# Kernel tuning notes

Measured on AMD Instinct MI355X. Metric: run time of the kernel, lower is better.

## Reference

```python
import jax, jax.numpy as jnp
import numpy as np

B, D, O, E, H, K = 4096, 1024, 1024, 8, 4096, 2


def setup_inputs() -> dict:
    key = jax.random.key(0)
    ks = jax.random.split(key, 5)
    scale_g = 1.0 / np.sqrt(D)
    scale_1 = 1.0 / np.sqrt(D)
    scale_2 = 1.0 / np.sqrt(H)
    return {
        "x": jax.random.normal(ks[0], (B, D), jnp.float32),
        "gate_w": jax.random.normal(ks[1], (D, E), jnp.float32) * scale_g,
        "gate_b": jnp.zeros((E,), jnp.float32),
        "w1": jax.random.normal(ks[2], (E, D, H), jnp.float32) * scale_1,
        "b1": jnp.zeros((E, H), jnp.float32),
        "w2": jax.random.normal(ks[3], (E, H, O), jnp.float32) * scale_2,
        "b2": jnp.zeros((E, O), jnp.float32),
    }


def reference(x, gate_w, gate_b, w1, b1, w2, b2):
    # Router: top-k logits, softmax over the k selected logits only
    logits = x @ gate_w + gate_b                      # [B, E]
    top_vals, top_idx = jax.lax.top_k(logits, K)      # [B, K]
    routing_w = jax.nn.softmax(top_vals, axis=-1)     # [B, K]

    # Dense all-expert MLP (grouped GEMM), then gather the k selected outputs
    h = jax.nn.relu(jnp.einsum("bd,edh->beh", x, w1) + b1)  # [B, E, H]
    y = jnp.einsum("beh,eho->beo", h, w2) + b2              # [B, E, O]
    sel = jnp.take_along_axis(y, top_idx[:, :, None], axis=1)  # [B, K, O]
    return jnp.sum(routing_w[:, :, None] * sel, axis=1)        # [B, O]
```

## Files before the change

kernel.cpp:

```cpp
#include <hip/hip_runtime.h>
#include <stdint.h>

typedef short bf16x8 __attribute__((ext_vector_type(8)));
typedef float f32x4  __attribute__((ext_vector_type(4)));

constexpr int BT = 4096;
constexpr int DD = 1024;
constexpr int OO = 1024;
constexpr int EE = 8;
constexpr int HH = 4096;
constexpr int SLOTS = 2 * BT;

constexpr int BM = 128, BN = 128, BK = 32;
constexpr int A_USH = BM * BK;
constexpr int SLOT_USH = (BM + BN) * BK;
constexpr int MTS = 32;
constexpr int G1_BLKS = 8 * 32 * MTS;
constexpr int G2_BLKS = 8 * 2 * 8 * MTS;

__device__ __forceinline__ unsigned short f2bf(float f) {
  unsigned u = __float_as_uint(f);
  u += 0x7fffu + ((u >> 16) & 1u);
  return (unsigned short)(u >> 16);
}

__device__ __forceinline__ void glds16(const unsigned short* g, unsigned short* l) {
  __builtin_amdgcn_global_load_lds(
      (const __attribute__((address_space(1))) void*)g,
      (__attribute__((address_space(3))) void*)l, 16, 0, 0);
}

__device__ __forceinline__ void cvt_body(const float* __restrict__ src,
                                         unsigned short* __restrict__ dst,
                                         int R, int C, int e, int r0, int c0, int t,
                                         unsigned short (*tile)[66]) {
  const float* s = src + (size_t)e * R * C;
  unsigned short* d = dst + (size_t)e * R * C;
#pragma unroll
  for (int p = 0; p < 4; ++p) {
    int ch = p * 256 + t;
    int rr = ch >> 4, cc = (ch & 15) << 2;
    float4 v = *(const float4*)&s[(size_t)(r0 + rr) * C + c0 + cc];
    unsigned lo = (unsigned)f2bf(v.x) | ((unsigned)f2bf(v.y) << 16);
    unsigned hi = (unsigned)f2bf(v.z) | ((unsigned)f2bf(v.w) << 16);
    *(uint2*)&tile[rr][cc] = make_uint2(lo, hi);
  }
  __syncthreads();
#pragma unroll
  for (int p = 0; p < 4; ++p) {
    int ch = p * 256 + t;
    int cc = ch >> 4, rr = (ch & 15) << 2;
    unsigned short v0 = tile[rr + 0][cc];
    unsigned short v1 = tile[rr + 1][cc];
    unsigned short v2 = tile[rr + 2][cc];
    unsigned short v3 = tile[rr + 3][cc];
    unsigned lo = (unsigned)v0 | ((unsigned)v1 << 16);
    unsigned hi = (unsigned)v2 | ((unsigned)v3 << 16);
    *(uint2*)&d[(size_t)(c0 + cc) * R + r0 + rr] = make_uint2(lo, hi);
  }
}

__global__ __launch_bounds__(256) void fusedA_k(const float* __restrict__ x,
                                                const float* __restrict__ gw,
                                                const float* __restrict__ gb,
                                                const float* __restrict__ w1,
                                                unsigned short* __restrict__ xb,
                                                int* __restrict__ cnt,
                                                int* __restrict__ list,
                                                float* __restrict__ rw,
                                                unsigned short* __restrict__ w1t) {
  __shared__ unsigned short tile[64][66];
  int bid = blockIdx.x;
  if (bid >= 1024) {
    int idx = bid - 1024;
    int e = idx >> 10, rem = idx & 1023;
    int r0 = (rem & 15) << 6, c0 = (rem >> 4) << 6;
    cvt_body(w1, w1t, DD, HH, e, r0, c0, threadIdx.x, tile);
    return;
  }
  int wave = threadIdx.x >> 6, lane = threadIdx.x & 63;
  int b = bid * 4 + wave;
  const float* xrow = x + (size_t)b * DD;
  float acc[8];
#pragma unroll
  for (int e = 0; e < 8; ++e) acc[e] = 0.f;
#pragma unroll
  for (int i = 0; i < 4; ++i) {
    int d0 = i * 256 + lane * 4;
    float4 v = *(const float4*)&xrow[d0];
    unsigned lo = (unsigned)f2bf(v.x) | ((unsigned)f2bf(v.y) << 16);
    unsigned hi = (unsigned)f2bf(v.z) | ((unsigned)f2bf(v.w) << 16);
    *(uint2*)&xb[(size_t)b * DD + d0] = make_uint2(lo, hi);
    const float* g0 = &gw[(size_t)d0 * 8];
    float fv[4] = {v.x, v.y, v.z, v.w};
#pragma unroll
    for (int q = 0; q < 4; ++q) {
      float4 ga = *(const float4*)&g0[q * 8];
      float4 gc = *(const float4*)&g0[q * 8 + 4];
      acc[0] += fv[q] * ga.x; acc[1] += fv[q] * ga.y;
      acc[2] += fv[q] * ga.z; acc[3] += fv[q] * ga.w;
      acc[4] += fv[q] * gc.x; acc[5] += fv[q] * gc.y;
      acc[6] += fv[q] * gc.z; acc[7] += fv[q] * gc.w;
    }
  }
#pragma unroll
  for (int off = 32; off > 0; off >>= 1) {
#pragma unroll
    for (int e = 0; e < 8; ++e) acc[e] += __shfl_down(acc[e], off);
  }
  if (lane == 0) {
    float v[8];
#pragma unroll
    for (int e = 0; e < 8; ++e) v[e] = acc[e] + gb[e];
    int i0 = 0;
#pragma unroll
    for (int e = 1; e < 8; ++e) if (v[e] > v[i0]) i0 = e;
    int i1 = (i0 == 0) ? 1 : 0;
#pragma unroll
    for (int e = 0; e < 8; ++e) if (e != i0 && v[e] > v[i1]) i1 = e;
    float e1 = __expf(v[i1] - v[i0]);
    float inv = 1.0f / (1.0f + e1);
    int p0 = atomicAdd(&cnt[i0], 1);
    list[i0 * BT + p0] = 2 * b;     rw[2 * b]     = inv;
    int p1 = atomicAdd(&cnt[i1], 1);
    list[i1 * BT + p1] = 2 * b + 1; rw[2 * b + 1] = e1 * inv;
  }
}

__global__ void tilemap_k(const int* __restrict__ cnt, int* __restrict__ tmap,
                          int* __restrict__ ntiles, int* __restrict__ tstart) {
  if (threadIdx.x == 0 && blockIdx.x == 0) {
    int t = 0, basewalk = 0;
    for (int e = 0; e < EE; ++e) {
      tstart[e] = t;
      int c = cnt[e];
      for (int m0 = 0; m0 < c; m0 += BM) {
        tmap[4 * t] = e; tmap[4 * t + 1] = m0; tmap[4 * t + 2] = basewalk + m0; ++t;
      }
      basewalk += c;
    }
    tstart[EE] = t;
    *ntiles = t;
  }
}

__global__ __launch_bounds__(256) void cvt_t_k(const float* __restrict__ src,
                                               unsigned short* __restrict__ dst,
                                               int R, int C) {
  __shared__ unsigned short tile[64][66];
  cvt_body(src, dst, R, C, blockIdx.z, blockIdx.x << 6, blockIdx.y << 6,
           threadIdx.x, tile);
}

__global__ __launch_bounds__(256, 3) void fusedB_k(const unsigned short* __restrict__ xb,
                                                   const unsigned short* __restrict__ w1t,
                                                   const float* __restrict__ b1,
                                                   const int* __restrict__ cnt,
                                                   const int* __restrict__ list,
                                                   const int* __restrict__ tmap,
                                                   const int* __restrict__ tstart,
                                                   unsigned short* __restrict__ hc,
                                                   const float* __restrict__ w2,
                                                   unsigned short* __restrict__ w2t) {
  __shared__ __align__(16) unsigned short lds[3 * SLOT_USH];
  __shared__ int slotbuf[BM];
  int bid = blockIdx.x;
  if (bid >= G1_BLKS) {
    int idx = bid - G1_BLKS;
    int e = idx >> 10, rem = idx & 1023;
    int r0 = (rem & 63) << 6, c0 = (rem >> 6) << 6;
    cvt_body(w2, w2t, HH, OO, e, r0, c0, threadIdx.x,
             (unsigned short (*)[66])lds);
    return;
  }
  int q = bid & 7, r = bid >> 3;
  int mts = r & (MTS - 1), nt = r >> 5;
  int tc0 = tstart[q];
  if (tc0 + mts >= tstart[q + 1]) return;
  int ti = tc0 + mts;
  int e = tmap[4 * ti], m0 = tmap[4 * ti + 1], base = tmap[4 * ti + 2];
  int cnt_e = cnt[e];
  int n0 = nt * BN;

  int t = threadIdx.x;
  if (t < BM) {
    int rr = m0 + t;
    slotbuf[t] = list[e * BT + (rr < cnt_e ? rr : 0)];
  }
  __syncthreads();

  int w = t >> 6, l = t & 63, lm = l & 15, lq = l >> 4;
  int wm = (w >> 1) * 64, wn = (w & 1) * 64;

  const unsigned short* aS[2];
  const unsigned short* bS[2];
  int dA[2], dB[2];
#pragma unroll
  for (int j = 0; j < 2; ++j) {
    int row = w * 32 + j * 16 + (l >> 2);
    int sch = ((l & 3) ^ ((row >> 1) & 3)) * 8;
    aS[j] = xb + (size_t)(slotbuf[row] >> 1) * DD + sch;
    bS[j] = w1t + (size_t)e * HH * DD + (size_t)(n0 + row) * DD + sch;
    dA[j] = w * 1024 + j * 512;
    dB[j] = A_USH + w * 1024 + j * 512;
  }

  int xs = (lq ^ ((lm >> 1) & 3)) * 8;
  int afo[4], bfo[4];
#pragma unroll
  for (int mi = 0; mi < 4; ++mi) afo[mi] = (wm + mi * 16 + lm) * BK + xs;
#pragma unroll
  for (int ni = 0; ni < 4; ++ni) bfo[ni] = A_USH + (wn + ni * 16 + lm) * BK + xs;

  f32x4 acc[4][4];
#pragma unroll
  for (int mi = 0; mi < 4; ++mi)
#pragma unroll
    for (int ni = 0; ni < 4; ++ni) acc[mi][ni] = f32x4{0.f, 0.f, 0.f, 0.f};

  constexpr int NT = DD / BK;

#pragma unroll
  for (int p = 0; p < 2; ++p) {
    unsigned short* Lb = lds + p * SLOT_USH;
    glds16(aS[0] + p * BK, Lb + dA[0]);
    glds16(aS[1] + p * BK, Lb + dA[1]);
    glds16(bS[0] + p * BK, Lb + dB[0]);
    glds16(bS[1] + p * BK, Lb + dB[1]);
  }
  asm volatile("s_waitcnt vmcnt(4)" ::: "memory");
  __builtin_amdgcn_s_barrier();
  asm volatile("" ::: "memory");

  int sc = 0, ss = 2;
  for (int tt = 0; tt < NT; ++tt) {
    {
      int ts = tt + 2;
      int ko = (ts < NT ? ts : NT - 1) * BK;
      unsigned short* Lb = lds + ss * SLOT_USH;
      glds16(aS[0] + ko, Lb + dA[0]);
      glds16(aS[1] + ko, Lb + dA[1]);
      glds16(bS[0] + ko, Lb + dB[0]);
      glds16(bS[1] + ko, Lb + dB[1]);
    }
    const unsigned short* Lc = lds + sc * SLOT_USH;
    bf16x8 af[4], bf[4];
#pragma unroll
    for (int mi = 0; mi < 4; ++mi) af[mi] = *(const bf16x8*)&Lc[afo[mi]];
#pragma unroll
    for (int ni = 0; ni < 4; ++ni) bf[ni] = *(const bf16x8*)&Lc[bfo[ni]];
    __builtin_amdgcn_s_setprio(1);
#pragma unroll
    for (int mi = 0; mi < 4; ++mi)
#pragma unroll
      for (int ni = 0; ni < 4; ++ni)
        acc[mi][ni] = __builtin_amdgcn_mfma_f32_16x16x32_bf16(af[mi], bf[ni], acc[mi][ni], 0, 0, 0);
    __builtin_amdgcn_s_setprio(0);
    asm volatile("s_waitcnt vmcnt(4)" ::: "memory");
    __builtin_amdgcn_s_barrier();
    asm volatile("" ::: "memory");
    if (++sc == 3) sc = 0;
    if (++ss == 3) ss = 0;
  }

  asm volatile("s_waitcnt vmcnt(0)" ::: "memory");
  __builtin_amdgcn_s_barrier();
  asm volatile("" ::: "memory");
  unsigned short* cb = lds + w * 4096;
  float bias[4];
#pragma unroll
  for (int ni = 0; ni < 4; ++ni) bias[ni] = b1[e * HH + n0 + wn + ni * 16 + lm];
#pragma unroll
  for (int mi = 0; mi < 4; ++mi)
#pragma unroll
    for (int ni = 0; ni < 4; ++ni)
#pragma unroll
      for (int rr = 0; rr < 4; ++rr)
        cb[(mi * 16 + lq * 4 + rr) * 64 + ni * 16 + lm] =
            f2bf(fmaxf(acc[mi][ni][rr] + bias[ni], 0.0f));
  asm volatile("s_waitcnt lgkmcnt(0)" ::: "memory");
#pragma unroll
  for (int it = 0; it < 8; ++it) {
    int rr = it * 8 + (l >> 3), chk = l & 7;
    int grow = wm + rr;
    if (m0 + grow < cnt_e) {
      uint4 v = *(const uint4*)&cb[rr * 64 + chk * 8];
      *(uint4*)&hc[(size_t)(base + grow) * HH + n0 + wn + chk * 8] = v;
    }
  }
}

__global__ __launch_bounds__(256, 3) void gemm2_k(const unsigned short* __restrict__ hc,
                                                  const unsigned short* __restrict__ w2t,
                                                  const float* __restrict__ b2,
                                                  const int* __restrict__ cnt,
                                                  const int* __restrict__ list,
                                                  const int* __restrict__ tmap,
                                                  const int* __restrict__ tstart,
                                                  const float* __restrict__ rw,
                                                  float* __restrict__ ybuf,
                                                  float* __restrict__ out) {
  int q = blockIdx.x & 7, r = blockIdx.x >> 3;
  int z = r >> 8, s = r & 255;
  int mts = s & (MTS - 1), nt = s >> 5;
  int tc0 = tstart[q];
  if (tc0 + mts >= tstart[q + 1]) return;
  int ti = tc0 + mts;
  int e = tmap[4 * ti], m0 = tmap[4 * ti + 1], base = tmap[4 * ti + 2];
  int cnt_e = cnt[e];
  int n0 = nt * BN;
  int kb0 = z * (HH / 2);
  constexpr int NT = (HH / 2) / BK;

  __shared__ __align__(16) unsigned short lds[3 * SLOT_USH];
  __shared__ int slotbuf[BM];
  __shared__ float rwbuf[BM];

  int t = threadIdx.x;
  if (t < BM) {
    int rr = m0 + t;
    int s_ = list[e * BT + (rr < cnt_e ? rr : 0)];
    slotbuf[t] = s_;
    rwbuf[t] = rw[s_];
  }
  __syncthreads();

  int w = t >> 6, l = t & 63, lm = l & 15, lq = l >> 4;
  int wm = (w >> 1) * 64, wn = (w & 1) * 64;

  const unsigned short* aS[2];
  const unsigned short* bS[2];
  int dA[2], dB[2];
#pragma unroll
  for (int j = 0; j < 2; ++j) {
    int row = w * 32 + j * 16 + (l >> 2);
    int sch = ((l & 3) ^ ((row >> 1) & 3)) * 8;
    int gr = base + row; if (gr > SLOTS - 1) gr = SLOTS - 1;
    aS[j] = hc + (size_t)gr * HH + kb0 + sch;
    bS[j] = w2t + (size_t)e * OO * HH + (size_t)(n0 + row) * HH + kb0 + sch;
    dA[j] = w * 1024 + j * 512;
    dB[j] = A_USH + w * 1024 + j * 512;
  }

  int xs = (lq ^ ((lm >> 1) & 3)) * 8;
  int afo[4], bfo[4];
#pragma unroll
  for (int mi = 0; mi < 4; ++mi) afo[mi] = (wm + mi * 16 + lm) * BK + xs;
#pragma unroll
  for (int ni = 0; ni < 4; ++ni) bfo[ni] = A_USH + (wn + ni * 16 + lm) * BK + xs;

  f32x4 acc[4][4];
#pragma unroll
  for (int mi = 0; mi < 4; ++mi)
#pragma unroll
    for (int ni = 0; ni < 4; ++ni) acc[mi][ni] = f32x4{0.f, 0.f, 0.f, 0.f};

#pragma unroll
  for (int p = 0; p < 2; ++p) {
    unsigned short* Lb = lds + p * SLOT_USH;
    glds16(aS[0] + p * BK, Lb + dA[0]);
    glds16(aS[1] + p * BK, Lb + dA[1]);
    glds16(bS[0] + p * BK, Lb + dB[0]);
    glds16(bS[1] + p * BK, Lb + dB[1]);
  }
  asm volatile("s_waitcnt vmcnt(4)" ::: "memory");
  __builtin_amdgcn_s_barrier();
  asm volatile("" ::: "memory");

  int sc = 0, ss = 2;
  for (int tt = 0; tt < NT; ++tt) {
    {
      int ts = tt + 2;
      int ko = (ts < NT ? ts : NT - 1) * BK;
      unsigned short* Lb = lds + ss * SLOT_USH;
      glds16(aS[0] + ko, Lb + dA[0]);
      glds16(aS[1] + ko, Lb + dA[1]);
      glds16(bS[0] + ko, Lb + dB[0]);
      glds16(bS[1] + ko, Lb + dB[1]);
    }
    const unsigned short* Lc = lds + sc * SLOT_USH;
    bf16x8 af[4], bf[4];
#pragma unroll
    for (int mi = 0; mi < 4; ++mi) af[mi] = *(const bf16x8*)&Lc[afo[mi]];
#pragma unroll
    for (int ni = 0; ni < 4; ++ni) bf[ni] = *(const bf16x8*)&Lc[bfo[ni]];
    __builtin_amdgcn_s_setprio(1);
#pragma unroll
    for (int mi = 0; mi < 4; ++mi)
#pragma unroll
      for (int ni = 0; ni < 4; ++ni)
        acc[mi][ni] = __builtin_amdgcn_mfma_f32_16x16x32_bf16(af[mi], bf[ni], acc[mi][ni], 0, 0, 0);
    __builtin_amdgcn_s_setprio(0);
    asm volatile("s_waitcnt vmcnt(4)" ::: "memory");
    __builtin_amdgcn_s_barrier();
    asm volatile("" ::: "memory");
    if (++sc == 3) sc = 0;
    if (++ss == 3) ss = 0;
  }
  asm volatile("s_waitcnt vmcnt(0)" ::: "memory");

  bool addb = (z == 0);
  size_t ybase = (size_t)z * SLOTS;
#pragma unroll
  for (int ni = 0; ni < 4; ++ni) {
    int ncol = n0 + wn + ni * 16 + lm;
    float bias = addb ? b2[e * OO + ncol] : 0.0f;
#pragma unroll
    for (int mi = 0; mi < 4; ++mi)
#pragma unroll
      for (int rr = 0; rr < 4; ++rr) {
        int lrow = wm + mi * 16 + lq * 4 + rr;
        if (m0 + lrow < cnt_e) {
          float v = (acc[mi][ni][rr] + bias) * rwbuf[lrow];
          int slot = slotbuf[lrow];
          if (ybuf) ybuf[(ybase + slot) * OO + ncol] = v;
          else      atomicAdd(&out[(size_t)(slot >> 1) * OO + ncol], v);
        }
      }
  }
}

__global__ __launch_bounds__(256) void combine_k(const float* __restrict__ y,
                                                 float* __restrict__ out, int nz) {
  int i = blockIdx.x * 256 + threadIdx.x;
  int b = i >> 8, c = i & 255;
  f32x4 acc = {0.f, 0.f, 0.f, 0.f};
  for (int z = 0; z < nz; ++z) {
#pragma unroll
    for (int k = 0; k < 2; ++k) {
      const float4 v = *(const float4*)&y[((size_t)z * SLOTS + 2 * b + k) * OO + c * 4];
      acc[0] += v.x; acc[1] += v.y; acc[2] += v.z; acc[3] += v.w;
    }
  }
  *(f32x4*)&out[(size_t)b * OO + c * 4] = acc;
}

extern "C" void kernel_launch(void* const* d_in, const int* in_sizes, int n_in,
                              void* d_out, int out_size, void* d_ws, size_t ws_size,
                              hipStream_t stream) {
  const float* x  = (const float*)d_in[0];
  const float* gw = (const float*)d_in[1];
  const float* gb = (const float*)d_in[2];
  const float* w1 = (const float*)d_in[3];
  const float* b1 = (const float*)d_in[4];
  const float* w2 = (const float*)d_in[5];
  const float* b2 = (const float*)d_in[6];
  float* out = (float*)d_out;
  char* ws = (char*)d_ws;

  int*            cnt    = (int*)(ws);
  int*            ntiles = (int*)(ws + 64);
  int*            tmap   = (int*)(ws + 128);
  int*            tstart = (int*)(ws + 2560);
  float*          rw     = (float*)(ws + 4096);
  int*            list   = (int*)(ws + (64u << 10));
  unsigned short* xb     = (unsigned short*)(ws + (1u  << 20));
  unsigned short* w1t    = (unsigned short*)(ws + (9u  << 20));

  bool roomy = ws_size >= (201u << 20);
  hipMemsetAsync(cnt, 0, 64, stream);

  if (roomy) {
    unsigned short* w2t = (unsigned short*)(ws + (73u  << 20));
    unsigned short* hc  = (unsigned short*)(ws + (137u << 20));
    float*          ybuf = (float*)(ws + (9u << 20));

    fusedA_k<<<1024 + 8192, 256, 0, stream>>>(x, gw, gb, w1, xb, cnt, list, rw, w1t);
    tilemap_k<<<1, 64, 0, stream>>>(cnt, tmap, ntiles, tstart);
    fusedB_k<<<G1_BLKS + 8192, 256, 0, stream>>>(xb, w1t, b1, cnt, list, tmap, tstart,
                                                 hc, w2, w2t);
    gemm2_k<<<G2_BLKS, 256, 0, stream>>>(hc, w2t, b2, cnt, list, tmap,
                                         tstart, rw, ybuf, out);
    combine_k<<<BT * OO / 1024, 256, 0, stream>>>(ybuf, out, 2);
  } else {
    if (ws_size < (137u << 20)) return;
    unsigned short* w2t = w1t;
    unsigned short* hc  = (unsigned short*)(ws + (73u << 20));
    hipMemsetAsync(out, 0, (size_t)BT * OO * sizeof(float), stream);
    fusedA_k<<<1024 + 8192, 256, 0, stream>>>(x, gw, gb, w1, xb, cnt, list, rw, w1t);
    tilemap_k<<<1, 64, 0, stream>>>(cnt, tmap, ntiles, tstart);
    fusedB_k<<<G1_BLKS, 256, 0, stream>>>(xb, w1t, b1, cnt, list, tmap, tstart,
                                          hc, w2, w2t);
    cvt_t_k<<<dim3(HH / 64, OO / 64, EE), 256, 0, stream>>>(w2, w2t, HH, OO);
    gemm2_k<<<G2_BLKS, 256, 0, stream>>>(hc, w2t, b2, cnt, list, tmap,
                                         tstart, rw, nullptr, out);
  }
}
```

Measured before the change: 642.8 us.

## Batch weight-convert blocks four tiles each and switch GEMMs to double buffering

Each weight-conversion block now handles four 64x64 tiles, issuing all 16 float4 loads up front before transposing through LDS. This cuts the conversion grid fourfold and puts more loads in flight per thread. Both grouped GEMM kernels drop from a three-slot LDS pipeline with prefetch distance two to a two-slot double buffer with vmcnt(0) waits, and raise launch bounds from 3 to 4 blocks per CU. The aim is higher occupancy from lower LDS use, at the cost of less latency hiding per wave and more register pressure in the converter.

Result: no change. 638.7 us (-0.6%).

```diff
diff --git a/kernel.cpp b/kernel.cpp
--- a/kernel.cpp
+++ b/kernel.cpp
@@ -30,33 +30,46 @@
       (__attribute__((address_space(3))) void*)l, 16, 0, 0);
 }
 
-__device__ __forceinline__ void cvt_body(const float* __restrict__ src,
-                                         unsigned short* __restrict__ dst,
-                                         int R, int C, int e, int r0, int c0, int t,
-                                         unsigned short (*tile)[66]) {
+__device__ __forceinline__ void cvt_body4(const float* __restrict__ src,
+                                          unsigned short* __restrict__ dst,
+                                          int R, int C, int e, int r0, int c0, int t,
+                                          unsigned short (*tile)[66]) {
   const float* s = src + (size_t)e * R * C;
   unsigned short* d = dst + (size_t)e * R * C;
-#pragma unroll
-  for (int p = 0; p < 4; ++p) {
-    int ch = p * 256 + t;
-    int rr = ch >> 4, cc = (ch & 15) << 2;
-    float4 v = *(const float4*)&s[(size_t)(r0 + rr) * C + c0 + cc];
-    unsigned lo = (unsigned)f2bf(v.x) | ((unsigned)f2bf(v.y) << 16);
-    unsigned hi = (unsigned)f2bf(v.z) | ((unsigned)f2bf(v.w) << 16);
-    *(uint2*)&tile[rr][cc] = make_uint2(lo, hi);
-  }
-  __syncthreads();
-#pragma unroll
-  for (int p = 0; p < 4; ++p) {
-    int ch = p * 256 + t;
-    int cc = ch >> 4, rr = (ch & 15) << 2;
-    unsigned short v0 = tile[rr + 0][cc];
-    unsigned short v1 = tile[rr + 1][cc];
-    unsigned short v2 = tile[rr + 2][cc];
-    unsigned short v3 = tile[rr + 3][cc];
-    unsigned lo = (unsigned)v0 | ((unsigned)v1 << 16);
-    unsigned hi = (unsigned)v2 | ((unsigned)v3 << 16);
-    *(uint2*)&d[(size_t)(c0 + cc) * R + r0 + rr] = make_uint2(lo, hi);
+  float4 v[16];
+#pragma unroll
+  for (int u = 0; u < 4; ++u)
+#pragma unroll
+    for (int p = 0; p < 4; ++p) {
+      int ch = p * 256 + t;
+      int rr = ch >> 4, cc = (ch & 15) << 2;
+      v[u * 4 + p] = *(const float4*)&s[(size_t)(r0 + rr) * C + c0 + u * 64 + cc];
+    }
+#pragma unroll
+  for (int u = 0; u < 4; ++u) {
+#pragma unroll
+    for (int p = 0; p < 4; ++p) {
+      int ch = p * 256 + t;
+      int rr = ch >> 4, cc = (ch & 15) << 2;
+      float4 q = v[u * 4 + p];
+      unsigned lo = (unsigned)f2bf(q.x) | ((unsigned)f2bf(q.y) << 16);
+      unsigned hi = (unsigned)f2bf(q.z) | ((unsigned)f2bf(q.w) << 16);
+      *(uint2*)&tile[rr][cc] = make_uint2(lo, hi);
+    }
+    __syncthreads();
+#pragma unroll
+    for (int p = 0; p < 4; ++p) {
+      int ch = p * 256 + t;
+      int cc = ch >> 4, rr = (ch & 15) << 2;
+      unsigned short v0 = tile[rr + 0][cc];
+      unsigned short v1 = tile[rr + 1][cc];
+      unsigned short v2 = tile[rr + 2][cc];
+      unsigned short v3 = tile[rr + 3][cc];
+      unsigned lo = (unsigned)v0 | ((unsigned)v1 << 16);
+      unsigned hi = (unsigned)v2 | ((unsigned)v3 << 16);
+      *(uint2*)&d[(size_t)(c0 + u * 64 + cc) * R + r0 + rr] = make_uint2(lo, hi);
+    }
+    __syncthreads();
   }
 }
 
@@ -73,9 +86,9 @@
   int bid = blockIdx.x;
   if (bid >= 1024) {
     int idx = bid - 1024;
-    int e = idx >> 10, rem = idx & 1023;
-    int r0 = (rem & 15) << 6, c0 = (rem >> 4) << 6;
-    cvt_body(w1, w1t, DD, HH, e, r0, c0, threadIdx.x, tile);
+    int e = idx >> 8, rem = idx & 255;
+    int r0 = (rem & 15) << 6, c0 = (rem >> 4) << 8;
+    cvt_body4(w1, w1t, DD, HH, e, r0, c0, threadIdx.x, tile);
     return;
   }
   int wave = threadIdx.x >> 6, lane = threadIdx.x & 63;
@@ -148,11 +161,11 @@
                                                unsigned short* __restrict__ dst,
                                                int R, int C) {
   __shared__ unsigned short tile[64][66];
-  cvt_body(src, dst, R, C, blockIdx.z, blockIdx.x << 6, blockIdx.y << 6,
-           threadIdx.x, tile);
-}
-
-__global__ __launch_bounds__(256, 3) void fusedB_k(const unsigned short* __restrict__ xb,
+  cvt_body4(src, dst, R, C, blockIdx.z, blockIdx.x << 6, blockIdx.y << 8,
+            threadIdx.x, tile);
+}
+
+__global__ __launch_bounds__(256, 4) void fusedB_k(const unsigned short* __restrict__ xb,
                                                    const unsigned short* __restrict__ w1t,
                                                    const float* __restrict__ b1,
                                                    const int* __restrict__ cnt,
@@ -162,15 +175,15 @@
                                                    unsigned short* __restrict__ hc,
                                                    const float* __restrict__ w2,
                                                    unsigned short* __restrict__ w2t) {
-  __shared__ __align__(16) unsigned short lds[3 * SLOT_USH];
+  __shared__ __align__(16) unsigned short lds[2 * SLOT_USH];
   __shared__ int slotbuf[BM];
   int bid = blockIdx.x;
   if (bid >= G1_BLKS) {
     int idx = bid - G1_BLKS;
-    int e = idx >> 10, rem = idx & 1023;
-    int r0 = (rem & 63) << 6, c0 = (rem >> 6) << 6;
-    cvt_body(w2, w2t, HH, OO, e, r0, c0, threadIdx.x,
-             (unsigned short (*)[66])lds);
+    int e = idx >> 8, rem = idx & 255;
+    int r0 = (rem & 63) << 6, c0 = (rem >> 6) << 8;
+    cvt_body4(w2, w2t, HH, OO, e, r0, c0, threadIdx.x,
+              (unsigned short (*)[66])lds);
     return;
   }
   int q = bid & 7, r = bid >> 3;
@@ -220,30 +233,24 @@
 
   constexpr int NT = DD / BK;
 
-#pragma unroll
-  for (int p = 0; p < 2; ++p) {
-    unsigned short* Lb = lds + p * SLOT_USH;
-    glds16(aS[0] + p * BK, Lb + dA[0]);
-    glds16(aS[1] + p * BK, Lb + dA[1]);
-    glds16(bS[0] + p * BK, Lb + dB[0]);
-    glds16(bS[1] + p * BK, Lb + dB[1]);
-  }
-  asm volatile("s_waitcnt vmcnt(4)" ::: "memory");
+  {
+    unsigned short* Lb = lds;
+    glds16(aS[0], Lb + dA[0]); glds16(aS[1], Lb + dA[1]);
+    glds16(bS[0], Lb + dB[0]); glds16(bS[1], Lb + dB[1]);
+  }
+  asm volatile("s_waitcnt vmcnt(0)" ::: "memory");
   __builtin_amdgcn_s_barrier();
   asm volatile("" ::: "memory");
 
-  int sc = 0, ss = 2;
   for (int tt = 0; tt < NT; ++tt) {
     {
-      int ts = tt + 2;
+      int ts = tt + 1;
       int ko = (ts < NT ? ts : NT - 1) * BK;
-      unsigned short* Lb = lds + ss * SLOT_USH;
-      glds16(aS[0] + ko, Lb + dA[0]);
-      glds16(aS[1] + ko, Lb + dA[1]);
-      glds16(bS[0] + ko, Lb + dB[0]);
-      glds16(bS[1] + ko, Lb + dB[1]);
-    }
-    const unsigned short* Lc = lds + sc * SLOT_USH;
+      unsigned short* Lb = lds + (ts & 1) * SLOT_USH;
+      glds16(aS[0] + ko, Lb + dA[0]); glds16(aS[1] + ko, Lb + dA[1]);
+      glds16(bS[0] + ko, Lb + dB[0]); glds16(bS[1] + ko, Lb + dB[1]);
+    }
+    const unsigned short* Lc = lds + (tt & 1) * SLOT_USH;
     bf16x8 af[4], bf[4];
 #pragma unroll
     for (int mi = 0; mi < 4; ++mi) af[mi] = *(const bf16x8*)&Lc[afo[mi]];
@@ -256,16 +263,11 @@
       for (int ni = 0; ni < 4; ++ni)
         acc[mi][ni] = __builtin_amdgcn_mfma_f32_16x16x32_bf16(af[mi], bf[ni], acc[mi][ni], 0, 0, 0);
     __builtin_amdgcn_s_setprio(0);
-    asm volatile("s_waitcnt vmcnt(4)" ::: "memory");
+    asm volatile("s_waitcnt vmcnt(0)" ::: "memory");
     __builtin_amdgcn_s_barrier();
     asm volatile("" ::: "memory");
-    if (++sc == 3) sc = 0;
-    if (++ss == 3) ss = 0;
-  }
-
-  asm volatile("s_waitcnt vmcnt(0)" ::: "memory");
-  __builtin_amdgcn_s_barrier();
-  asm volatile("" ::: "memory");
+  }
+
   unsigned short* cb = lds + w * 4096;
   float bias[4];
 #pragma unroll
@@ -290,7 +292,7 @@
   }
 }
 
-__global__ __launch_bounds__(256, 3) void gemm2_k(const unsigned short* __restrict__ hc,
+__global__ __launch_bounds__(256, 4) void gemm2_k(const unsigned short* __restrict__ hc,
                                                   const unsigned short* __restrict__ w2t,
                                                   const float* __restrict__ b2,
                                                   const int* __restrict__ cnt,
@@ -312,7 +314,7 @@
   int kb0 = z * (HH / 2);
   constexpr int NT = (HH / 2) / BK;
 
-  __shared__ __align__(16) unsigned short lds[3 * SLOT_USH];
+  __shared__ __align__(16) unsigned short lds[2 * SLOT_USH];
   __shared__ int slotbuf[BM];
   __shared__ float rwbuf[BM];
 
@@ -355,30 +357,24 @@
 #pragma unroll
     for (int ni = 0; ni < 4; ++ni) acc[mi][ni] = f32x4{0.f, 0.f, 0.f, 0.f};
 
-#pragma unroll
-  for (int p = 0; p < 2; ++p) {
-    unsigned short* Lb = lds + p * SLOT_USH;
-    glds16(aS[0] + p * BK, Lb + dA[0]);
-    glds16(aS[1] + p * BK, Lb + dA[1]);
-    glds16(bS[0] + p * BK, Lb + dB[0]);
-    glds16(bS[1] + p * BK, Lb + dB[1]);
-  }
-  asm volatile("s_waitcnt vmcnt(4)" ::: "memory");
+  {
+    unsigned short* Lb = lds;
+    glds16(aS[0], Lb + dA[0]); glds16(aS[1], Lb + dA[1]);
+    glds16(bS[0], Lb + dB[0]); glds16(bS[1], Lb + dB[1]);
+  }
+  asm volatile("s_waitcnt vmcnt(0)" ::: "memory");
   __builtin_amdgcn_s_barrier();
   asm volatile("" ::: "memory");
 
-  int sc = 0, ss = 2;
   for (int tt = 0; tt < NT; ++tt) {
     {
-      int ts = tt + 2;
+      int ts = tt + 1;
       int ko = (ts < NT ? ts : NT - 1) * BK;
-      unsigned short* Lb = lds + ss * SLOT_USH;
-      glds16(aS[0] + ko, Lb + dA[0]);
-      glds16(aS[1] + ko, Lb + dA[1]);
-      glds16(bS[0] + ko, Lb + dB[0]);
-      glds16(bS[1] + ko, Lb + dB[1]);
-    }
-    const unsigned short* Lc = lds + sc * SLOT_USH;
+      unsigned short* Lb = lds + (ts & 1) * SLOT_USH;
+      glds16(aS[0] + ko, Lb + dA[0]); glds16(aS[1] + ko, Lb + dA[1]);
+      glds16(bS[0] + ko, Lb + dB[0]); glds16(bS[1] + ko, Lb + dB[1]);
+    }
+    const unsigned short* Lc = lds + (tt & 1) * SLOT_USH;
     bf16x8 af[4], bf[4];
 #pragma unroll
     for (int mi = 0; mi < 4; ++mi) af[mi] = *(const bf16x8*)&Lc[afo[mi]];
@@ -391,13 +387,10 @@
       for (int ni = 0; ni < 4; ++ni)
         acc[mi][ni] = __builtin_amdgcn_mfma_f32_16x16x32_bf16(af[mi], bf[ni], acc[mi][ni], 0, 0, 0);
     __builtin_amdgcn_s_setprio(0);
-    asm volatile("s_waitcnt vmcnt(4)" ::: "memory");
+    asm volatile("s_waitcnt vmcnt(0)" ::: "memory");
     __builtin_amdgcn_s_barrier();
     asm volatile("" ::: "memory");
-    if (++sc == 3) sc = 0;
-    if (++ss == 3) ss = 0;
-  }
-  asm volatile("s_waitcnt vmcnt(0)" ::: "memory");
+  }
 
   bool addb = (z == 0);
   size_t ybase = (size_t)z * SLOTS;
@@ -465,9 +458,9 @@
     unsigned short* hc  = (unsigned short*)(ws + (137u << 20));
     float*          ybuf = (float*)(ws + (9u << 20));
 
-    fusedA_k<<<1024 + 8192, 256, 0, stream>>>(x, gw, gb, w1, xb, cnt, list, rw, w1t);
+    fusedA_k<<<1024 + 2048, 256, 0, stream>>>(x, gw, gb, w1, xb, cnt, list, rw, w1t);
     tilemap_k<<<1, 64, 0, stream>>>(cnt, tmap, ntiles, tstart);
-    fusedB_k<<<G1_BLKS + 8192, 256, 0, stream>>>(xb, w1t, b1, cnt, list, tmap, tstart,
+    fusedB_k<<<G1_BLKS + 2048, 256, 0, stream>>>(xb, w1t, b1, cnt, list, tmap, tstart,
                                                  hc, w2, w2t);
     gemm2_k<<<G2_BLKS, 256, 0, stream>>>(hc, w2t, b2, cnt, list, tmap,
                                          tstart, rw, ybuf, out);
@@ -477,11 +470,11 @@
     unsigned short* w2t = w1t;
     unsigned short* hc  = (unsigned short*)(ws + (73u << 20));
     hipMemsetAsync(out, 0, (size_t)BT * OO * sizeof(float), stream);
-    fusedA_k<<<1024 + 8192, 256, 0, stream>>>(x, gw, gb, w1, xb, cnt, list, rw, w1t);
+    fusedA_k<<<1024 + 2048, 256, 0, stream>>>(x, gw, gb, w1, xb, cnt, list, rw, w1t);
     tilemap_k<<<1, 64, 0, stream>>>(cnt, tmap, ntiles, tstart);
     fusedB_k<<<G1_BLKS, 256, 0, stream>>>(xb, w1t, b1, cnt, list, tmap, tstart,
                                           hc, w2, w2t);
-    cvt_t_k<<<dim3(HH / 64, OO / 64, EE), 256, 0, stream>>>(w2, w2t, HH, OO);
+    cvt_t_k<<<dim3(HH / 64, OO / 256, EE), 256, 0, stream>>>(w2, w2t, HH, OO);
     gemm2_k<<<G2_BLKS, 256, 0, stream>>>(hc, w2t, b2, cnt, list, tmap,
                                          tstart, rw, nullptr, out);
   }
```
